# Performance work log

Measured on AMD Instinct MI355X. Metric: run time of the kernel, lower is better.

Reference implementation:

```python
import jax, jax.numpy as jnp
import numpy as np

N_NODES = 50000
N_EDGES = 800000


def _glorot(key, shape):
    fan_in, fan_out = shape
    lim = float(np.sqrt(6.0 / (fan_in + fan_out)))
    return jax.random.uniform(key, shape, jnp.float32, -lim, lim)


def setup_inputs() -> dict:
    key = jax.random.key(0)
    ks = jax.random.split(key, 8)
    x = jax.random.normal(ks[0], (N_NODES, 2), jnp.float32)
    edge_index = jax.random.randint(ks[1], (2, N_EDGES), 0, N_NODES, jnp.int64)
    edge_weight = jax.random.uniform(ks[2], (N_EDGES,), jnp.float32)
    return {
        "x": x,
        "edge_index": edge_index,
        "edge_weight": edge_weight,
        "W1": _glorot(ks[3], (2, 128)),
        "b1": jnp.zeros((128,), jnp.float32),
        "W2": _glorot(ks[4], (128, 64)),
        "b2": jnp.zeros((64,), jnp.float32),
        "W3": _glorot(ks[5], (64, 1)),
        "b3": jnp.zeros((1,), jnp.float32),
    }


def _gcn_conv(x, W, b, src, dst, ew, n_nodes):
    # PyG GCNConv with normalize=False: out[i] = sum_{e:(j->i)} ew[e] * (x_j @ W) + b
    h = x @ W                       # [N, F_out] tiny GEMM
    msg = h[src] * ew[:, None]      # [E, F_out] gather + scale
    out = jax.ops.segment_sum(msg, dst, num_segments=n_nodes)  # scatter-add
    return out + b


def reference(x, edge_index, edge_weight, W1, b1, W2, b2, W3, b3):
    src, dst = edge_index[0], edge_index[1]  # source_to_target flow: aggregate at dst
    n = x.shape[0]
    h1 = jax.nn.relu(_gcn_conv(x, W1, b1, src, dst, edge_weight, n))
    # dropout is a no-op in eval mode
    h2 = jax.nn.relu(_gcn_conv(h1, W2, b2, src, dst, edge_weight, n))
    h3 = _gcn_conv(h2, W3, b3, src, dst, edge_weight, n)  # [N, 1]
    return h3.squeeze(-1)  # [N]
```

## Files before the change

### kernel.cpp

```cpp
#include <hip/hip_runtime.h>
#include <hip/hip_fp16.h>

#define N_NODES 50000
#define N_EDGES 800000
#define BSHIFT 7
#define NBKT ((N_NODES + 127) >> BSHIFT)
#define CAP 4096
#define P1_EDGES 2048
#define P1_BLOCKS ((N_EDGES + P1_EDGES - 1) / P1_EDGES)
#define BIN_THREADS 512
#define SORT_THREADS 512
#define SORT_LDS_CAP 3072

__global__ void bin_edges(const int* __restrict__ src, const int* __restrict__ dst,
                          const float* __restrict__ ew, int* __restrict__ bcur,
                          unsigned* __restrict__ bpk, unsigned char* __restrict__ bdl) {
    __shared__ unsigned spk[P1_EDGES];
    __shared__ unsigned short sdst[P1_EDGES];
    __shared__ int cnt[NBKT];
    __shared__ int cbase[NBKT];
    int t = threadIdx.x;
    if (t < NBKT) cnt[t] = 0;
    __syncthreads();
    int e0 = blockIdx.x * P1_EDGES;
    for (int k = 0; k < P1_EDGES / BIN_THREADS; k++) {
        int i = k * BIN_THREADS + t;
        int e = e0 + i;
        if (e < N_EDGES) {
            int d = dst[e];
            unsigned hw = (unsigned)__half_as_ushort(__float2half(ew[e]));
            spk[i] = (unsigned)src[e] | (hw << 16);
            sdst[i] = (unsigned short)d;
            atomicAdd(&cnt[d >> BSHIFT], 1);
        }
    }
    __syncthreads();
    if (t < NBKT) {
        int v = cnt[t];
        int base = v ? atomicAdd(&bcur[t], v) : 0;
        cbase[t] = t * CAP + base;
        cnt[t] = 0;
    }
    __syncthreads();
    int nmax = N_EDGES - e0;
    if (nmax > P1_EDGES) nmax = P1_EDGES;
    for (int k = 0; k < P1_EDGES / BIN_THREADS; k++) {
        int i = k * BIN_THREADS + t;
        if (i < nmax) {
            int d = sdst[i];
            int b = d >> BSHIFT;
            int pos = cbase[b] + atomicAdd(&cnt[b], 1);
            bpk[pos] = spk[i];
            bdl[pos] = (unsigned char)(d & 127);
        }
    }
}

__global__ void sort_bucket(const int* __restrict__ bcur, const unsigned* __restrict__ bpk,
                            const unsigned char* __restrict__ bdl,
                            unsigned* __restrict__ sorted, int2* __restrict__ rowspan) {
    __shared__ unsigned spk[SORT_LDS_CAP];
    __shared__ unsigned short sdl[SORT_LDS_CAP];
    __shared__ int nh[128];
    __shared__ int scn[128];
    __shared__ int lcur[128];
    int b = blockIdx.x;
    int t = threadIdx.x;
    int base = b * CAP;
    int n = bcur[b];
    if (n > CAP) n = CAP;
    bool lds_path = (n <= SORT_LDS_CAP);
    if (t < 128) nh[t] = 0;
    __syncthreads();
    if (lds_path) {
        for (int e = t; e < n; e += SORT_THREADS) {
            spk[e] = bpk[base + e];
            unsigned short d = bdl[base + e];
            sdl[e] = d;
            atomicAdd(&nh[d], 1);
        }
    } else {
        for (int e = t; e < n; e += SORT_THREADS)
            atomicAdd(&nh[bdl[base + e]], 1);
    }
    __syncthreads();
    int v = 0;
    if (t < 128) { v = nh[t]; scn[t] = v; }
    __syncthreads();
    for (int off = 1; off < 128; off <<= 1) {
        int u = (t < 128 && t >= off) ? scn[t - off] : 0;
        __syncthreads();
        if (t < 128) scn[t] += u;
        __syncthreads();
    }
    if (t < 128) {
        int ex = scn[t] - v;
        int node = (b << BSHIFT) + t;
        if (node < N_NODES) rowspan[node] = make_int2(base + ex, base + ex + v);
        nh[t] = ex;
        lcur[t] = 0;
    }
    __syncthreads();
    if (lds_path) {
        for (int e = t; e < n; e += SORT_THREADS) {
            int dlow = sdl[e];
            int pos = base + nh[dlow] + atomicAdd(&lcur[dlow], 1);
            sorted[pos] = spk[e];
        }
    } else {
        for (int e = t; e < n; e += SORT_THREADS) {
            int dlow = bdl[base + e];
            int pos = base + nh[dlow] + atomicAdd(&lcur[dlow], 1);
            sorted[pos] = bpk[base + e];
        }
    }
}

__device__ __forceinline__ float edge_w(unsigned p) {
    return __half2float(__ushort_as_half((unsigned short)(p >> 16)));
}

#define L1_NODES_PER_BLOCK 32
__global__ void fused_l1(const int2* __restrict__ rowspan, const unsigned* __restrict__ sorted,
                         const float* __restrict__ x, const float* __restrict__ W1,
                         const float* __restrict__ b1, const float* __restrict__ W2,
                         __half* __restrict__ t2) {
    __shared__ float w2s[128 * 64];
    __shared__ float hls[4][8][128];
    for (int k = threadIdx.x; k < 128 * 64; k += 256) w2s[k] = W2[k];
    int wave = threadIdx.x >> 6;
    int lane = threadIdx.x & 63;
    float w1a = W1[lane],      w1b = W1[128 + lane];
    float w1c = W1[64 + lane], w1d = W1[192 + lane];
    float b1lo = b1[lane], b1hi = b1[64 + lane];
    __syncthreads();

    int sub = lane >> 4;
    int sl  = lane & 15;
    int base = blockIdx.x * L1_NODES_PER_BLOCK + wave * 8;

#pragma unroll
    for (int g = 0; g < 2; g++) {
        int gnode = base + g * 4 + sub;
        float a0 = 0.f, a1 = 0.f;
        if (gnode < N_NODES) {
            int2 sp = rowspan[gnode];
            for (int e = sp.x + sl; e < sp.y; e += 16) {
                unsigned p = sorted[e];
                float w = edge_w(p);
                float2 xv = ((const float2*)x)[p & 0xFFFF];
                a0 = fmaf(w, xv.x, a0);
                a1 = fmaf(w, xv.y, a1);
            }
        }
#pragma unroll
        for (int off = 1; off < 16; off <<= 1) {
            a0 += __shfl_xor(a0, off);
            a1 += __shfl_xor(a1, off);
        }
#pragma unroll
        for (int n = 0; n < 4; n++) {
            float an0 = __shfl(a0, 16 * n);
            float an1 = __shfl(a1, 16 * n);
            float hlo = fmaxf(fmaf(an0, w1a, fmaf(an1, w1b, b1lo)), 0.f);
            float hhi = fmaxf(fmaf(an0, w1c, fmaf(an1, w1d, b1hi)), 0.f);
            hls[wave][g * 4 + n][lane] = hlo;
            hls[wave][g * 4 + n][64 + lane] = hhi;
        }
    }
    float acc[8] = {0.f, 0.f, 0.f, 0.f, 0.f, 0.f, 0.f, 0.f};
#pragma unroll 2
    for (int k4 = 0; k4 < 32; k4++) {
        float w0 = w2s[(4 * k4 + 0) * 64 + lane];
        float w1 = w2s[(4 * k4 + 1) * 64 + lane];
        float w2 = w2s[(4 * k4 + 2) * 64 + lane];
        float w3 = w2s[(4 * k4 + 3) * 64 + lane];
#pragma unroll
        for (int n = 0; n < 8; n++) {
            float4 h = *(const float4*)&hls[wave][n][4 * k4];
            acc[n] = fmaf(h.x, w0, fmaf(h.y, w1, fmaf(h.z, w2, fmaf(h.w, w3, acc[n]))));
        }
    }
#pragma unroll
    for (int n = 0; n < 8; n++)
        if (base + n < N_NODES) t2[(base + n) * 64 + lane] = __float2half(acc[n]);
}

__global__ void gather2_dot3(const int2* __restrict__ rowspan, const unsigned* __restrict__ sorted,
                             const __half* __restrict__ t2, const float* __restrict__ b2,
                             const float* __restrict__ W3, float* __restrict__ t3) {
    int gtid = blockIdx.x * blockDim.x + threadIdx.x;
    int node = gtid >> 6;
    int lane = threadIdx.x & 63;
    if (node >= N_NODES) return;
    int eg  = lane >> 3;
    int fli = lane & 7;
    int2 sp = rowspan[node];
    float a0 = 0.f, a1 = 0.f, a2 = 0.f, a3 = 0.f, a4 = 0.f, a5 = 0.f, a6 = 0.f, a7 = 0.f;
    int e = sp.x + eg;
    for (; e + 8 < sp.y; e += 16) {
        unsigned p0 = sorted[e];
        unsigned p1 = sorted[e + 8];
        uint4 q0 = *(const uint4*)(t2 + (p0 & 0xFFFF) * 64 + fli * 8);
        uint4 q1 = *(const uint4*)(t2 + (p1 & 0xFFFF) * 64 + fli * 8);
        float w0 = edge_w(p0), w1 = edge_w(p1);
        float2 f;
        f = __half22float2(*(const __half2*)&q0.x); a0 = fmaf(w0, f.x, a0); a1 = fmaf(w0, f.y, a1);
        f = __half22float2(*(const __half2*)&q0.y); a2 = fmaf(w0, f.x, a2); a3 = fmaf(w0, f.y, a3);
        f = __half22float2(*(const __half2*)&q0.z); a4 = fmaf(w0, f.x, a4); a5 = fmaf(w0, f.y, a5);
        f = __half22float2(*(const __half2*)&q0.w); a6 = fmaf(w0, f.x, a6); a7 = fmaf(w0, f.y, a7);
        f = __half22float2(*(const __half2*)&q1.x); a0 = fmaf(w1, f.x, a0); a1 = fmaf(w1, f.y, a1);
        f = __half22float2(*(const __half2*)&q1.y); a2 = fmaf(w1, f.x, a2); a3 = fmaf(w1, f.y, a3);
        f = __half22float2(*(const __half2*)&q1.z); a4 = fmaf(w1, f.x, a4); a5 = fmaf(w1, f.y, a5);
        f = __half22float2(*(const __half2*)&q1.w); a6 = fmaf(w1, f.x, a6); a7 = fmaf(w1, f.y, a7);
    }
    if (e < sp.y) {
        unsigned p = sorted[e];
        uint4 q = *(const uint4*)(t2 + (p & 0xFFFF) * 64 + fli * 8);
        float w = edge_w(p);
        float2 f;
        f = __half22float2(*(const __half2*)&q.x); a0 = fmaf(w, f.x, a0); a1 = fmaf(w, f.y, a1);
        f = __half22float2(*(const __half2*)&q.y); a2 = fmaf(w, f.x, a2); a3 = fmaf(w, f.y, a3);
        f = __half22float2(*(const __half2*)&q.z); a4 = fmaf(w, f.x, a4); a5 = fmaf(w, f.y, a5);
        f = __half22float2(*(const __half2*)&q.w); a6 = fmaf(w, f.x, a6); a7 = fmaf(w, f.y, a7);
    }
#pragma unroll
    for (int off = 8; off < 64; off <<= 1) {
        a0 += __shfl_xor(a0, off); a1 += __shfl_xor(a1, off);
        a2 += __shfl_xor(a2, off); a3 += __shfl_xor(a3, off);
        a4 += __shfl_xor(a4, off); a5 += __shfl_xor(a5, off);
        a6 += __shfl_xor(a6, off); a7 += __shfl_xor(a7, off);
    }
    float4 bA = *(const float4*)(b2 + fli * 8);
    float4 bB = *(const float4*)(b2 + fli * 8 + 4);
    float4 wA = *(const float4*)(W3 + fli * 8);
    float4 wB = *(const float4*)(W3 + fli * 8 + 4);
    float h = fmaxf(a0 + bA.x, 0.f) * wA.x + fmaxf(a1 + bA.y, 0.f) * wA.y +
              fmaxf(a2 + bA.z, 0.f) * wA.z + fmaxf(a3 + bA.w, 0.f) * wA.w +
              fmaxf(a4 + bB.x, 0.f) * wB.x + fmaxf(a5 + bB.y, 0.f) * wB.y +
              fmaxf(a6 + bB.z, 0.f) * wB.z + fmaxf(a7 + bB.w, 0.f) * wB.w;
#pragma unroll
    for (int off = 1; off < 8; off <<= 1) h += __shfl_xor(h, off);
    if (lane == 0) t3[node] = h;
}

__global__ void gather3(const int2* __restrict__ rowspan, const unsigned* __restrict__ sorted,
                        const float* __restrict__ t3, const float* __restrict__ b3,
                        float* __restrict__ out) {
    int gtid = blockIdx.x * blockDim.x + threadIdx.x;
    int wid = gtid >> 6;
    int lane = threadIdx.x & 63;
    int sub = lane >> 4;
    int sl  = lane & 15;
    int node = wid * 4 + sub;
    if (node >= N_NODES) return;
    int2 sp = rowspan[node];
    float acc = 0.f;
    for (int e = sp.x + sl; e < sp.y; e += 16) {
        unsigned p = sorted[e];
        acc = fmaf(edge_w(p), t3[p & 0xFFFF], acc);
    }
#pragma unroll
    for (int off = 1; off < 16; off <<= 1) acc += __shfl_xor(acc, off);
    if (sl == 0) out[node] = acc + b3[0];
}

extern "C" void kernel_launch(void* const* d_in, const int* in_sizes, int n_in,
                              void* d_out, int out_size, void* d_ws, size_t ws_size,
                              hipStream_t stream) {
    const float* x  = (const float*)d_in[0];
    const int*   ei = (const int*)d_in[1];
    const float* ew = (const float*)d_in[2];
    const float* W1 = (const float*)d_in[3];
    const float* b1 = (const float*)d_in[4];
    const float* W2 = (const float*)d_in[5];
    const float* b2 = (const float*)d_in[6];
    const float* W3 = (const float*)d_in[7];
    const float* b3 = (const float*)d_in[8];
    float* out = (float*)d_out;

    const int* src = ei;
    const int* dst = ei + N_EDGES;

    char* p = (char*)d_ws;
    int*  bcur    = (int*)p;            p += NBKT * sizeof(int);
    p = (char*)(((uintptr_t)p + 15) & ~(uintptr_t)15);
    int2* rowspan = (int2*)p;           p += N_NODES * sizeof(int2);
    unsigned* bpk = (unsigned*)p;       p += (long)NBKT * CAP * sizeof(unsigned);
    unsigned char* bdl = (unsigned char*)p; p += (long)NBKT * CAP;
    p = (char*)(((uintptr_t)p + 15) & ~(uintptr_t)15);
    unsigned* sorted  = (unsigned*)p;   p += (long)NBKT * CAP * sizeof(unsigned);
    __half* t2    = (__half*)p;         p += 64L * N_NODES * sizeof(__half);
    float* t3     = (float*)p;          p += N_NODES * sizeof(float);

    hipMemsetAsync(bcur, 0, NBKT * sizeof(int), stream);

    bin_edges<<<P1_BLOCKS, BIN_THREADS, 0, stream>>>(src, dst, ew, bcur, bpk, bdl);
    sort_bucket<<<NBKT, SORT_THREADS, 0, stream>>>(bcur, bpk, bdl, sorted, rowspan);

    fused_l1<<<(N_NODES + L1_NODES_PER_BLOCK - 1) / L1_NODES_PER_BLOCK, 256, 0, stream>>>(
        rowspan, sorted, x, W1, b1, W2, t2);

    gather2_dot3<<<(N_NODES * 64 + 255) / 256, 256, 0, stream>>>(rowspan, sorted, t2, b2, W3, t3);

    gather3<<<((N_NODES + 3) / 4 * 64 + 255) / 256, 256, 0, stream>>>(rowspan, sorted, t3, b3, out);
}
```

Baseline: 165.3 us.

## Fuse all GCN stages into one persistent cooperative kernel with grid syncs

Replaces the memset and the five kernel launches (bin, bucket sort, fused layer 1, layer 2 gather, layer 3 gather) with one cooperative persistent kernel of 512 blocks. The stages are separated by grid.sync and each block loops over its share of chunks, buckets or nodes. The aim is to remove launch gaps and per-kernel ramp-up and drain costs. In exchange, each stage now runs with fewer threads per block (256 instead of 512 for binning and sorting) and a fixed grid size, and every grid barrier adds its own cost. The layer 1 W2 product now works on 4 nodes per pass instead of 8, and W2 is reloaded into LDS on every call.

```diff
diff --git a/kernel.cpp b/kernel.cpp
--- a/kernel.cpp
+++ b/kernel.cpp
@@ -1,275 +1,298 @@
 #include <hip/hip_runtime.h>
 #include <hip/hip_fp16.h>
+#include <hip/hip_cooperative_groups.h>
+
+namespace cg = cooperative_groups;
 
 #define N_NODES 50000
 #define N_EDGES 800000
 #define BSHIFT 7
 #define NBKT ((N_NODES + 127) >> BSHIFT)
 #define CAP 4096
-#define P1_EDGES 2048
-#define P1_BLOCKS ((N_EDGES + P1_EDGES - 1) / P1_EDGES)
-#define BIN_THREADS 512
-#define SORT_THREADS 512
+#define CHUNK 2048
+#define NCHUNK ((N_EDGES + CHUNK - 1) / CHUNK)
 #define SORT_LDS_CAP 3072
-
-__global__ void bin_edges(const int* __restrict__ src, const int* __restrict__ dst,
-                          const float* __restrict__ ew, int* __restrict__ bcur,
-                          unsigned* __restrict__ bpk, unsigned char* __restrict__ bdl) {
-    __shared__ unsigned spk[P1_EDGES];
-    __shared__ unsigned short sdst[P1_EDGES];
-    __shared__ int cnt[NBKT];
-    __shared__ int cbase[NBKT];
-    int t = threadIdx.x;
-    if (t < NBKT) cnt[t] = 0;
-    __syncthreads();
-    int e0 = blockIdx.x * P1_EDGES;
-    for (int k = 0; k < P1_EDGES / BIN_THREADS; k++) {
-        int i = k * BIN_THREADS + t;
-        int e = e0 + i;
-        if (e < N_EDGES) {
-            int d = dst[e];
-            unsigned hw = (unsigned)__half_as_ushort(__float2half(ew[e]));
-            spk[i] = (unsigned)src[e] | (hw << 16);
-            sdst[i] = (unsigned short)d;
-            atomicAdd(&cnt[d >> BSHIFT], 1);
-        }
-    }
-    __syncthreads();
-    if (t < NBKT) {
-        int v = cnt[t];
-        int base = v ? atomicAdd(&bcur[t], v) : 0;
-        cbase[t] = t * CAP + base;
-        cnt[t] = 0;
-    }
-    __syncthreads();
-    int nmax = N_EDGES - e0;
-    if (nmax > P1_EDGES) nmax = P1_EDGES;
-    for (int k = 0; k < P1_EDGES / BIN_THREADS; k++) {
-        int i = k * BIN_THREADS + t;
-        if (i < nmax) {
-            int d = sdst[i];
-            int b = d >> BSHIFT;
-            int pos = cbase[b] + atomicAdd(&cnt[b], 1);
-            bpk[pos] = spk[i];
-            bdl[pos] = (unsigned char)(d & 127);
-        }
-    }
-}
-
-__global__ void sort_bucket(const int* __restrict__ bcur, const unsigned* __restrict__ bpk,
-                            const unsigned char* __restrict__ bdl,
-                            unsigned* __restrict__ sorted, int2* __restrict__ rowspan) {
-    __shared__ unsigned spk[SORT_LDS_CAP];
-    __shared__ unsigned short sdl[SORT_LDS_CAP];
-    __shared__ int nh[128];
-    __shared__ int scn[128];
-    __shared__ int lcur[128];
-    int b = blockIdx.x;
-    int t = threadIdx.x;
-    int base = b * CAP;
-    int n = bcur[b];
-    if (n > CAP) n = CAP;
-    bool lds_path = (n <= SORT_LDS_CAP);
-    if (t < 128) nh[t] = 0;
-    __syncthreads();
-    if (lds_path) {
-        for (int e = t; e < n; e += SORT_THREADS) {
-            spk[e] = bpk[base + e];
-            unsigned short d = bdl[base + e];
-            sdl[e] = d;
-            atomicAdd(&nh[d], 1);
-        }
-    } else {
-        for (int e = t; e < n; e += SORT_THREADS)
-            atomicAdd(&nh[bdl[base + e]], 1);
-    }
-    __syncthreads();
-    int v = 0;
-    if (t < 128) { v = nh[t]; scn[t] = v; }
-    __syncthreads();
-    for (int off = 1; off < 128; off <<= 1) {
-        int u = (t < 128 && t >= off) ? scn[t - off] : 0;
-        __syncthreads();
-        if (t < 128) scn[t] += u;
-        __syncthreads();
-    }
-    if (t < 128) {
-        int ex = scn[t] - v;
-        int node = (b << BSHIFT) + t;
-        if (node < N_NODES) rowspan[node] = make_int2(base + ex, base + ex + v);
-        nh[t] = ex;
-        lcur[t] = 0;
-    }
-    __syncthreads();
-    if (lds_path) {
-        for (int e = t; e < n; e += SORT_THREADS) {
-            int dlow = sdl[e];
-            int pos = base + nh[dlow] + atomicAdd(&lcur[dlow], 1);
-            sorted[pos] = spk[e];
-        }
-    } else {
-        for (int e = t; e < n; e += SORT_THREADS) {
-            int dlow = bdl[base + e];
-            int pos = base + nh[dlow] + atomicAdd(&lcur[dlow], 1);
-            sorted[pos] = bpk[base + e];
-        }
-    }
-}
+#define G_BLOCKS 512
+#define THREADS 256
 
 __device__ __forceinline__ float edge_w(unsigned p) {
     return __half2float(__ushort_as_half((unsigned short)(p >> 16)));
 }
 
-#define L1_NODES_PER_BLOCK 32
-__global__ void fused_l1(const int2* __restrict__ rowspan, const unsigned* __restrict__ sorted,
-                         const float* __restrict__ x, const float* __restrict__ W1,
-                         const float* __restrict__ b1, const float* __restrict__ W2,
-                         __half* __restrict__ t2) {
-    __shared__ float w2s[128 * 64];
-    __shared__ float hls[4][8][128];
-    for (int k = threadIdx.x; k < 128 * 64; k += 256) w2s[k] = W2[k];
-    int wave = threadIdx.x >> 6;
-    int lane = threadIdx.x & 63;
-    float w1a = W1[lane],      w1b = W1[128 + lane];
-    float w1c = W1[64 + lane], w1d = W1[192 + lane];
-    float b1lo = b1[lane], b1hi = b1[64 + lane];
-    __syncthreads();
-
-    int sub = lane >> 4;
-    int sl  = lane & 15;
-    int base = blockIdx.x * L1_NODES_PER_BLOCK + wave * 8;
-
-#pragma unroll
-    for (int g = 0; g < 2; g++) {
-        int gnode = base + g * 4 + sub;
-        float a0 = 0.f, a1 = 0.f;
-        if (gnode < N_NODES) {
-            int2 sp = rowspan[gnode];
-            for (int e = sp.x + sl; e < sp.y; e += 16) {
+__global__ __launch_bounds__(THREADS, 4) void gcn_all(
+    const int* __restrict__ src, const int* __restrict__ dst, const float* __restrict__ ew,
+    const float* __restrict__ x, const float* __restrict__ W1, const float* __restrict__ b1,
+    const float* __restrict__ W2, const float* __restrict__ b2, const float* __restrict__ W3,
+    const float* __restrict__ b3, int* __restrict__ bcur, unsigned* __restrict__ bpk,
+    unsigned char* __restrict__ bdl, unsigned* __restrict__ sorted, int2* __restrict__ rowspan,
+    __half* __restrict__ t2, float* __restrict__ t3, float* __restrict__ out) {
+    cg::grid_group grid = cg::this_grid();
+    __shared__ __align__(16) char smem[40960];
+    int t = threadIdx.x;
+    int wave = t >> 6;
+    int lane = t & 63;
+
+    for (int i = blockIdx.x * THREADS + t; i < NBKT; i += gridDim.x * THREADS) bcur[i] = 0;
+    grid.sync();
+
+    {
+        unsigned* spk = (unsigned*)smem;
+        unsigned short* sd = (unsigned short*)(smem + 8192);
+        int* cnt = (int*)(smem + 12288);
+        int* cbase = (int*)(smem + 13852);
+        for (int c = blockIdx.x; c < NCHUNK; c += gridDim.x) {
+            for (int i = t; i < NBKT; i += THREADS) cnt[i] = 0;
+            __syncthreads();
+            int e0 = c * CHUNK;
+            for (int k = 0; k < CHUNK / THREADS; k++) {
+                int i = k * THREADS + t;
+                int e = e0 + i;
+                if (e < N_EDGES) {
+                    int d = dst[e];
+                    unsigned hw = (unsigned)__half_as_ushort(__float2half(ew[e]));
+                    spk[i] = (unsigned)src[e] | (hw << 16);
+                    sd[i] = (unsigned short)d;
+                    atomicAdd(&cnt[d >> BSHIFT], 1);
+                }
+            }
+            __syncthreads();
+            for (int i = t; i < NBKT; i += THREADS) {
+                int v = cnt[i];
+                int base = v ? atomicAdd(&bcur[i], v) : 0;
+                cbase[i] = i * CAP + base;
+                cnt[i] = 0;
+            }
+            __syncthreads();
+            int nmax = N_EDGES - e0;
+            if (nmax > CHUNK) nmax = CHUNK;
+            for (int k = 0; k < CHUNK / THREADS; k++) {
+                int i = k * THREADS + t;
+                if (i < nmax) {
+                    int d = sd[i];
+                    int b = d >> BSHIFT;
+                    int pos = cbase[b] + atomicAdd(&cnt[b], 1);
+                    bpk[pos] = spk[i];
+                    bdl[pos] = (unsigned char)(d & 127);
+                }
+            }
+            __syncthreads();
+        }
+    }
+    grid.sync();
+
+    {
+        unsigned* spk = (unsigned*)smem;
+        unsigned short* sdl = (unsigned short*)(smem + 12288);
+        int* nh = (int*)(smem + 18432);
+        int* scn = (int*)(smem + 18944);
+        int* lcur = (int*)(smem + 19456);
+        for (int b = blockIdx.x; b < NBKT; b += gridDim.x) {
+            int base = b * CAP;
+            int n = bcur[b];
+            if (n > CAP) n = CAP;
+            bool lds_path = (n <= SORT_LDS_CAP);
+            if (t < 128) nh[t] = 0;
+            __syncthreads();
+            if (lds_path) {
+                for (int e = t; e < n; e += THREADS) {
+                    spk[e] = bpk[base + e];
+                    unsigned short d = bdl[base + e];
+                    sdl[e] = d;
+                    atomicAdd(&nh[d], 1);
+                }
+            } else {
+                for (int e = t; e < n; e += THREADS)
+                    atomicAdd(&nh[bdl[base + e]], 1);
+            }
+            __syncthreads();
+            int v = 0;
+            if (t < 128) { v = nh[t]; scn[t] = v; }
+            __syncthreads();
+            for (int off = 1; off < 128; off <<= 1) {
+                int u = (t < 128 && t >= off) ? scn[t - off] : 0;
+                __syncthreads();
+                if (t < 128) scn[t] += u;
+                __syncthreads();
+            }
+            if (t < 128) {
+                int ex = scn[t] - v;
+                int node = (b << BSHIFT) + t;
+                if (node < N_NODES) rowspan[node] = make_int2(base + ex, base + ex + v);
+                nh[t] = ex;
+                lcur[t] = 0;
+            }
+            __syncthreads();
+            if (lds_path) {
+                for (int e = t; e < n; e += THREADS) {
+                    int dlow = sdl[e];
+                    int pos = base + nh[dlow] + atomicAdd(&lcur[dlow], 1);
+                    sorted[pos] = spk[e];
+                }
+            } else {
+                for (int e = t; e < n; e += THREADS) {
+                    int dlow = bdl[base + e];
+                    int pos = base + nh[dlow] + atomicAdd(&lcur[dlow], 1);
+                    sorted[pos] = bpk[base + e];
+                }
+            }
+            __syncthreads();
+        }
+    }
+    grid.sync();
+
+    {
+        float* w2s = (float*)smem;
+        float* hls = (float*)(smem + 32768);
+        for (int k = t; k < 128 * 64; k += THREADS) w2s[k] = W2[k];
+        float w1a = W1[lane],      w1b = W1[128 + lane];
+        float w1c = W1[64 + lane], w1d = W1[192 + lane];
+        float b1lo = b1[lane], b1hi = b1[64 + lane];
+        __syncthreads();
+        int sub = lane >> 4;
+        int sl  = lane & 15;
+        float* hw = hls + wave * 4 * 128;
+        const int NGROUP = (N_NODES + 31) / 32;
+        for (int gidx = blockIdx.x; gidx < NGROUP; gidx += gridDim.x) {
+            int nb = gidx * 32 + wave * 8;
+#pragma unroll
+            for (int g = 0; g < 2; g++) {
+                int base4 = nb + g * 4;
+                int gnode = base4 + sub;
+                float a0 = 0.f, a1 = 0.f;
+                if (gnode < N_NODES) {
+                    int2 sp = rowspan[gnode];
+                    for (int e = sp.x + sl; e < sp.y; e += 16) {
+                        unsigned p = sorted[e];
+                        float w = edge_w(p);
+                        float2 xv = ((const float2*)x)[p & 0xFFFF];
+                        a0 = fmaf(w, xv.x, a0);
+                        a1 = fmaf(w, xv.y, a1);
+                    }
+                }
+#pragma unroll
+                for (int off = 1; off < 16; off <<= 1) {
+                    a0 += __shfl_xor(a0, off);
+                    a1 += __shfl_xor(a1, off);
+                }
+#pragma unroll
+                for (int nn = 0; nn < 4; nn++) {
+                    float an0 = __shfl(a0, 16 * nn);
+                    float an1 = __shfl(a1, 16 * nn);
+                    float hlo = fmaxf(fmaf(an0, w1a, fmaf(an1, w1b, b1lo)), 0.f);
+                    float hhi = fmaxf(fmaf(an0, w1c, fmaf(an1, w1d, b1hi)), 0.f);
+                    hw[nn * 128 + lane] = hlo;
+                    hw[nn * 128 + 64 + lane] = hhi;
+                }
+                float acc0 = 0.f, acc1 = 0.f, acc2 = 0.f, acc3 = 0.f;
+#pragma unroll 4
+                for (int k4 = 0; k4 < 32; k4++) {
+                    float w0 = w2s[(4 * k4 + 0) * 64 + lane];
+                    float w1 = w2s[(4 * k4 + 1) * 64 + lane];
+                    float w2 = w2s[(4 * k4 + 2) * 64 + lane];
+                    float w3 = w2s[(4 * k4 + 3) * 64 + lane];
+                    float4 h0 = *(const float4*)&hw[0 * 128 + 4 * k4];
+                    float4 h1 = *(const float4*)&hw[1 * 128 + 4 * k4];
+                    float4 h2 = *(const float4*)&hw[2 * 128 + 4 * k4];
+                    float4 h3 = *(const float4*)&hw[3 * 128 + 4 * k4];
+                    acc0 = fmaf(h0.x, w0, fmaf(h0.y, w1, fmaf(h0.z, w2, fmaf(h0.w, w3, acc0))));
+                    acc1 = fmaf(h1.x, w0, fmaf(h1.y, w1, fmaf(h1.z, w2, fmaf(h1.w, w3, acc1))));
+                    acc2 = fmaf(h2.x, w0, fmaf(h2.y, w1, fmaf(h2.z, w2, fmaf(h2.w, w3, acc2))));
+                    acc3 = fmaf(h3.x, w0, fmaf(h3.y, w1, fmaf(h3.z, w2, fmaf(h3.w, w3, acc3))));
+                }
+                if (base4 + 0 < N_NODES) t2[(base4 + 0) * 64 + lane] = __float2half(acc0);
+                if (base4 + 1 < N_NODES) t2[(base4 + 1) * 64 + lane] = __float2half(acc1);
+                if (base4 + 2 < N_NODES) t2[(base4 + 2) * 64 + lane] = __float2half(acc2);
+                if (base4 + 3 < N_NODES) t2[(base4 + 3) * 64 + lane] = __float2half(acc3);
+            }
+        }
+    }
+    grid.sync();
+
+    {
+        int eg  = lane >> 3;
+        int fli = lane & 7;
+        int stride = gridDim.x * 4;
+        for (int node = blockIdx.x * 4 + wave; node < N_NODES; node += stride) {
+            int2 sp = rowspan[node];
+            float a0 = 0.f, a1 = 0.f, a2 = 0.f, a3 = 0.f, a4 = 0.f, a5 = 0.f, a6 = 0.f, a7 = 0.f;
+            int e = sp.x + eg;
+            for (; e + 8 < sp.y; e += 16) {
+                unsigned p0 = sorted[e];
+                unsigned p1 = sorted[e + 8];
+                uint4 q0 = *(const uint4*)(t2 + (p0 & 0xFFFF) * 64 + fli * 8);
+                uint4 q1 = *(const uint4*)(t2 + (p1 & 0xFFFF) * 64 + fli * 8);
+                float w0 = edge_w(p0), w1 = edge_w(p1);
+                float2 f;
+                f = __half22float2(*(const __half2*)&q0.x); a0 = fmaf(w0, f.x, a0); a1 = fmaf(w0, f.y, a1);
+                f = __half22float2(*(const __half2*)&q0.y); a2 = fmaf(w0, f.x, a2); a3 = fmaf(w0, f.y, a3);
+                f = __half22float2(*(const __half2*)&q0.z); a4 = fmaf(w0, f.x, a4); a5 = fmaf(w0, f.y, a5);
+                f = __half22float2(*(const __half2*)&q0.w); a6 = fmaf(w0, f.x, a6); a7 = fmaf(w0, f.y, a7);
+                f = __half22float2(*(const __half2*)&q1.x); a0 = fmaf(w1, f.x, a0); a1 = fmaf(w1, f.y, a1);
+                f = __half22float2(*(const __half2*)&q1.y); a2 = fmaf(w1, f.x, a2); a3 = fmaf(w1, f.y, a3);
+                f = __half22float2(*(const __half2*)&q1.z); a4 = fmaf(w1, f.x, a4); a5 = fmaf(w1, f.y, a5);
+                f = __half22float2(*(const __half2*)&q1.w); a6 = fmaf(w1, f.x, a6); a7 = fmaf(w1, f.y, a7);
+            }
+            if (e < sp.y) {
                 unsigned p = sorted[e];
+                uint4 q = *(const uint4*)(t2 + (p & 0xFFFF) * 64 + fli * 8);
                 float w = edge_w(p);
-                float2 xv = ((const float2*)x)[p & 0xFFFF];
-                a0 = fmaf(w, xv.x, a0);
-                a1 = fmaf(w, xv.y, a1);
-            }
-        }
-#pragma unroll
-        for (int off = 1; off < 16; off <<= 1) {
-            a0 += __shfl_xor(a0, off);
-            a1 += __shfl_xor(a1, off);
-        }
-#pragma unroll
-        for (int n = 0; n < 4; n++) {
-            float an0 = __shfl(a0, 16 * n);
-            float an1 = __shfl(a1, 16 * n);
-            float hlo = fmaxf(fmaf(an0, w1a, fmaf(an1, w1b, b1lo)), 0.f);
-            float hhi = fmaxf(fmaf(an0, w1c, fmaf(an1, w1d, b1hi)), 0.f);
-            hls[wave][g * 4 + n][lane] = hlo;
-            hls[wave][g * 4 + n][64 + lane] = hhi;
-        }
-    }
-    float acc[8] = {0.f, 0.f, 0.f, 0.f, 0.f, 0.f, 0.f, 0.f};
-#pragma unroll 2
-    for (int k4 = 0; k4 < 32; k4++) {
-        float w0 = w2s[(4 * k4 + 0) * 64 + lane];
-        float w1 = w2s[(4 * k4 + 1) * 64 + lane];
-        float w2 = w2s[(4 * k4 + 2) * 64 + lane];
-        float w3 = w2s[(4 * k4 + 3) * 64 + lane];
-#pragma unroll
-        for (int n = 0; n < 8; n++) {
-            float4 h = *(const float4*)&hls[wave][n][4 * k4];
-            acc[n] = fmaf(h.x, w0, fmaf(h.y, w1, fmaf(h.z, w2, fmaf(h.w, w3, acc[n]))));
-        }
-    }
-#pragma unroll
-    for (int n = 0; n < 8; n++)
-        if (base + n < N_NODES) t2[(base + n) * 64 + lane] = __float2half(acc[n]);
-}
-
-__global__ void gather2_dot3(const int2* __restrict__ rowspan, const unsigned* __restrict__ sorted,
-                             const __half* __restrict__ t2, const float* __restrict__ b2,
-                             const float* __restrict__ W3, float* __restrict__ t3) {
-    int gtid = blockIdx.x * blockDim.x + threadIdx.x;
-    int node = gtid >> 6;
-    int lane = threadIdx.x & 63;
-    if (node >= N_NODES) return;
-    int eg  = lane >> 3;
-    int fli = lane & 7;
-    int2 sp = rowspan[node];
-    float a0 = 0.f, a1 = 0.f, a2 = 0.f, a3 = 0.f, a4 = 0.f, a5 = 0.f, a6 = 0.f, a7 = 0.f;
-    int e = sp.x + eg;
-    for (; e + 8 < sp.y; e += 16) {
-        unsigned p0 = sorted[e];
-        unsigned p1 = sorted[e + 8];
-        uint4 q0 = *(const uint4*)(t2 + (p0 & 0xFFFF) * 64 + fli * 8);
-        uint4 q1 = *(const uint4*)(t2 + (p1 & 0xFFFF) * 64 + fli * 8);
-        float w0 = edge_w(p0), w1 = edge_w(p1);
-        float2 f;
-        f = __half22float2(*(const __half2*)&q0.x); a0 = fmaf(w0, f.x, a0); a1 = fmaf(w0, f.y, a1);
-        f = __half22float2(*(const __half2*)&q0.y); a2 = fmaf(w0, f.x, a2); a3 = fmaf(w0, f.y, a3);
-        f = __half22float2(*(const __half2*)&q0.z); a4 = fmaf(w0, f.x, a4); a5 = fmaf(w0, f.y, a5);
-        f = __half22float2(*(const __half2*)&q0.w); a6 = fmaf(w0, f.x, a6); a7 = fmaf(w0, f.y, a7);
-        f = __half22float2(*(const __half2*)&q1.x); a0 = fmaf(w1, f.x, a0); a1 = fmaf(w1, f.y, a1);
-        f = __half22float2(*(const __half2*)&q1.y); a2 = fmaf(w1, f.x, a2); a3 = fmaf(w1, f.y, a3);
-        f = __half22float2(*(const __half2*)&q1.z); a4 = fmaf(w1, f.x, a4); a5 = fmaf(w1, f.y, a5);
-        f = __half22float2(*(const __half2*)&q1.w); a6 = fmaf(w1, f.x, a6); a7 = fmaf(w1, f.y, a7);
-    }
-    if (e < sp.y) {
-        unsigned p = sorted[e];
-        uint4 q = *(const uint4*)(t2 + (p & 0xFFFF) * 64 + fli * 8);
-        float w = edge_w(p);
-        float2 f;
-        f = __half22float2(*(const __half2*)&q.x); a0 = fmaf(w, f.x, a0); a1 = fmaf(w, f.y, a1);
-        f = __half22float2(*(const __half2*)&q.y); a2 = fmaf(w, f.x, a2); a3 = fmaf(w, f.y, a3);
-        f = __half22float2(*(const __half2*)&q.z); a4 = fmaf(w, f.x, a4); a5 = fmaf(w, f.y, a5);
-        f = __half22float2(*(const __half2*)&q.w); a6 = fmaf(w, f.x, a6); a7 = fmaf(w, f.y, a7);
-    }
-#pragma unroll
-    for (int off = 8; off < 64; off <<= 1) {
-        a0 += __shfl_xor(a0, off); a1 += __shfl_xor(a1, off);
-        a2 += __shfl_xor(a2, off); a3 += __shfl_xor(a3, off);
-        a4 += __shfl_xor(a4, off); a5 += __shfl_xor(a5, off);
-        a6 += __shfl_xor(a6, off); a7 += __shfl_xor(a7, off);
-    }
-    float4 bA = *(const float4*)(b2 + fli * 8);
-    float4 bB = *(const float4*)(b2 + fli * 8 + 4);
-    float4 wA = *(const float4*)(W3 + fli * 8);
-    float4 wB = *(const float4*)(W3 + fli * 8 + 4);
-    float h = fmaxf(a0 + bA.x, 0.f) * wA.x + fmaxf(a1 + bA.y, 0.f) * wA.y +
-              fmaxf(a2 + bA.z, 0.f) * wA.z + fmaxf(a3 + bA.w, 0.f) * wA.w +
-              fmaxf(a4 + bB.x, 0.f) * wB.x + fmaxf(a5 + bB.y, 0.f) * wB.y +
-              fmaxf(a6 + bB.z, 0.f) * wB.z + fmaxf(a7 + bB.w, 0.f) * wB.w;
-#pragma unroll
-    for (int off = 1; off < 8; off <<= 1) h += __shfl_xor(h, off);
-    if (lane == 0) t3[node] = h;
-}
-
-__global__ void gather3(const int2* __restrict__ rowspan, const unsigned* __restrict__ sorted,
-                        const float* __restrict__ t3, const float* __restrict__ b3,
-                        float* __restrict__ out) {
-    int gtid = blockIdx.x * blockDim.x + threadIdx.x;
-    int wid = gtid >> 6;
-    int lane = threadIdx.x & 63;
-    int sub = lane >> 4;
-    int sl  = lane & 15;
-    int node = wid * 4 + sub;
-    if (node >= N_NODES) return;
-    int2 sp = rowspan[node];
-    float acc = 0.f;
-    for (int e = sp.x + sl; e < sp.y; e += 16) {
-        unsigned p = sorted[e];
-        acc = fmaf(edge_w(p), t3[p & 0xFFFF], acc);
-    }
-#pragma unroll
-    for (int off = 1; off < 16; off <<= 1) acc += __shfl_xor(acc, off);
-    if (sl == 0) out[node] = acc + b3[0];
+                float2 f;
+                f = __half22float2(*(const __half2*)&q.x); a0 = fmaf(w, f.x, a0); a1 = fmaf(w, f.y, a1);
+                f = __half22float2(*(const __half2*)&q.y); a2 = fmaf(w, f.x, a2); a3 = fmaf(w, f.y, a3);
+                f = __half22float2(*(const __half2*)&q.z); a4 = fmaf(w, f.x, a4); a5 = fmaf(w, f.y, a5);
+                f = __half22float2(*(const __half2*)&q.w); a6 = fmaf(w, f.x, a6); a7 = fmaf(w, f.y, a7);
+            }
+#pragma unroll
+            for (int off = 8; off < 64; off <<= 1) {
+                a0 += __shfl_xor(a0, off); a1 += __shfl_xor(a1, off);
+                a2 += __shfl_xor(a2, off); a3 += __shfl_xor(a3, off);
+                a4 += __shfl_xor(a4, off); a5 += __shfl_xor(a5, off);
+                a6 += __shfl_xor(a6, off); a7 += __shfl_xor(a7, off);
+            }
+            float4 bA = *(const float4*)(b2 + fli * 8);
+            float4 bB = *(const float4*)(b2 + fli * 8 + 4);
+            float4 wA = *(const float4*)(W3 + fli * 8);
+            float4 wB = *(const float4*)(W3 + fli * 8 + 4);
+            float h = fmaxf(a0 + bA.x, 0.f) * wA.x + fmaxf(a1 + bA.y, 0.f) * wA.y +
+                      fmaxf(a2 + bA.z, 0.f) * wA.z + fmaxf(a3 + bA.w, 0.f) * wA.w +
+                      fmaxf(a4 + bB.x, 0.f) * wB.x + fmaxf(a5 + bB.y, 0.f) * wB.y +
+                      fmaxf(a6 + bB.z, 0.f) * wB.z + fmaxf(a7 + bB.w, 0.f) * wB.w;
+#pragma unroll
+            for (int off = 1; off < 8; off <<= 1) h += __shfl_xor(h, off);
+            if (lane == 0) t3[node] = h;
+        }
+    }
+    grid.sync();
+
+    {
+        int sub = lane >> 4;
+        int sl  = lane & 15;
+        int stride = gridDim.x * 4;
+        const int NWID = (N_NODES + 3) / 4;
+        for (int wid = blockIdx.x * 4 + wave; wid < NWID; wid += stride) {
+            int node = wid * 4 + sub;
+            float acc = 0.f;
+            if (node < N_NODES) {
+                int2 sp = rowspan[node];
+                for (int e = sp.x + sl; e < sp.y; e += 16) {
+                    unsigned p = sorted[e];
+                    acc = fmaf(edge_w(p), t3[p & 0xFFFF], acc);
+                }
+            }
+#pragma unroll
+            for (int off = 1; off < 16; off <<= 1) acc += __shfl_xor(acc, off);
+            if (sl == 0 && node < N_NODES) out[node] = acc + b3[0];
+        }
+    }
 }
 
 extern "C" void kernel_launch(void* const* d_in, const int* in_sizes, int n_in,
                               void* d_out, int out_size, void* d_ws, size_t ws_size,
                               hipStream_t stream) {
+    const int*   ei = (const int*)d_in[1];
+    const int* src = ei;
+    const int* dst = ei + N_EDGES;
     const float* x  = (const float*)d_in[0];
-    const int*   ei = (const int*)d_in[1];
     const float* ew = (const float*)d_in[2];
     const float* W1 = (const float*)d_in[3];
     const float* b1 = (const float*)d_in[4];
@@ -278,9 +301,6 @@
     const float* W3 = (const float*)d_in[7];
     const float* b3 = (const float*)d_in[8];
     float* out = (float*)d_out;
-
-    const int* src = ei;
-    const int* dst = ei + N_EDGES;
 
     char* p = (char*)d_ws;
     int*  bcur    = (int*)p;            p += NBKT * sizeof(int);
@@ -293,15 +313,11 @@
     __half* t2    = (__half*)p;         p += 64L * N_NODES * sizeof(__half);
     float* t3     = (float*)p;          p += N_NODES * sizeof(float);
 
-    hipMemsetAsync(bcur, 0, NBKT * sizeof(int), stream);
-
-    bin_edges<<<P1_BLOCKS, BIN_THREADS, 0, stream>>>(src, dst, ew, bcur, bpk, bdl);
-    sort_bucket<<<NBKT, SORT_THREADS, 0, stream>>>(bcur, bpk, bdl, sorted, rowspan);
-
-    fused_l1<<<(N_NODES + L1_NODES_PER_BLOCK - 1) / L1_NODES_PER_BLOCK, 256, 0, stream>>>(
-        rowspan, sorted, x, W1, b1, W2, t2);
-
-    gather2_dot3<<<(N_NODES * 64 + 255) / 256, 256, 0, stream>>>(rowspan, sorted, t2, b2, W3, t3);
-
-    gather3<<<((N_NODES + 3) / 4 * 64 + 255) / 256, 256, 0, stream>>>(rowspan, sorted, t3, b3, out);
+    void* args[] = {
+        (void*)&src, (void*)&dst, (void*)&ew, (void*)&x, (void*)&W1, (void*)&b1,
+        (void*)&W2, (void*)&b2, (void*)&W3, (void*)&b3, (void*)&bcur, (void*)&bpk,
+        (void*)&bdl, (void*)&sorted, (void*)&rowspan, (void*)&t2, (void*)&t3, (void*)&out
+    };
+    hipLaunchCooperativeKernel((const void*)gcn_all, dim3(G_BLOCKS), dim3(THREADS),
+                               args, 0, stream);
 }
```

After: 489.6 us. +196.2%, slower.
